# Optimization experiments

Hardware: AMD Instinct MI355X
Metric: run time of the kernel (lower is better)

Reference implementation:

```python
import jax, jax.numpy as jnp
import numpy as np

B, NP, NR = 4, 2048, 10
EDGE_F = 32
EMB = 64          # emb_features == out_features (required for layer stacking)
ESM_EMB = 64
HEADS = 16
NUM_LAYERS = 4
LN_EPS = 1e-5


def _ln(x, g, b):
    mu = jnp.mean(x, axis=-1, keepdims=True)
    var = jnp.var(x, axis=-1, keepdims=True)
    return (x - mu) / jnp.sqrt(var + LN_EPS) * g + b


def setup_inputs() -> dict:
    key = jax.random.key(0)
    ks = jax.random.split(key, 32)
    s = 0.05  # xavier-ish scale for weights
    inp = {
        "pep_feat": jax.random.normal(ks[0], (B, NP, 27 + 1280), jnp.float32),
        "rec_feat": jax.random.normal(ks[1], (B, NP, NR, 42 + 1280), jnp.float32),
        "edge_feat": jax.random.normal(ks[2], (B, NP, NR, EDGE_F), jnp.float32),
        # embedding weights (torch Linear convention: y = x @ W.T)
        "W_rec_esm": jax.random.normal(ks[3], (ESM_EMB, 1280), jnp.float32) * s,
        "W_pep_esm": jax.random.normal(ks[4], (ESM_EMB, 1280), jnp.float32) * s,
        "W_pep_emb": jax.random.normal(ks[5], (EMB, 27 + ESM_EMB), jnp.float32) * s,
        "W_rec_emb": jax.random.normal(ks[6], (EMB, 21 + ESM_EMB), jnp.float32) * s,
        "W_edge_emb": jax.random.normal(ks[7], (EMB, EDGE_F), jnp.float32) * s,
        "pep_ln_g": jnp.ones((EMB,), jnp.float32),
        "pep_ln_b": jnp.zeros((EMB,), jnp.float32),
        "rec_ln_g": jnp.ones((EMB,), jnp.float32),
        "rec_ln_b": jnp.zeros((EMB,), jnp.float32),
        # stacked GraphAttention layer params [L, ...]
        "ga_Wp": jax.random.normal(ks[8], (NUM_LAYERS, EMB, EMB), jnp.float32) * s,
        "ga_bp": jnp.zeros((NUM_LAYERS, EMB), jnp.float32),
        "ga_Wr": jax.random.normal(ks[9], (NUM_LAYERS, EMB, 2 * EMB), jnp.float32) * s,
        "ga_br": jnp.zeros((NUM_LAYERS, EMB), jnp.float32),
        "ga_Wv": jax.random.normal(ks[10], (NUM_LAYERS, EMB, 2 * EMB), jnp.float32) * s,
        "ga_bv": jnp.zeros((NUM_LAYERS, EMB), jnp.float32),
        # self-attention pooling: LN + MLP [64 -> 64 -> 32 -> 16 heads], no biases
        "pool_ln_g": jnp.ones((EMB,), jnp.float32),
        "pool_ln_b": jnp.zeros((EMB,), jnp.float32),
        "pool_W0": jax.random.normal(ks[11], (EMB, EMB), jnp.float32) * s,
        "pool_W1": jax.random.normal(ks[12], (EMB // 2, EMB), jnp.float32) * s,
        "pool_W2": jax.random.normal(ks[13], (HEADS, EMB // 2), jnp.float32) * s,
        # final projection
        "mlp_W": jax.random.normal(ks[14], (EMB // 2, EMB), jnp.float32) * s,
        "mlp_b": jnp.zeros((EMB // 2,), jnp.float32),
    }
    return inp


def _forward(pep_feat, rec_feat, edge_feat, W_rec_esm, W_pep_esm, W_pep_emb,
             W_rec_emb, W_edge_emb, pep_ln_g, pep_ln_b, rec_ln_g, rec_ln_b,
             ga_Wp, ga_bp, ga_Wr, ga_br, ga_Wv, ga_bv,
             pool_ln_g, pool_ln_b, pool_W0, pool_W1, pool_W2, mlp_W, mlp_b):
    # --- embeddings ---
    rec_esm = rec_feat[..., 42:] @ W_rec_esm.T                       # [B,NP,10,ESM]
    pep_esm = pep_feat[..., -1280:] @ W_pep_esm.T                    # [B,NP,ESM]
    rec = jnp.concatenate([rec_feat[..., :21], rec_esm], axis=-1) @ W_rec_emb.T
    pep = jnp.concatenate([pep_feat[..., :27], pep_esm], axis=-1) @ W_pep_emb.T
    edge = edge_feat @ W_edge_emb.T                                  # [B,NP,10,EMB]
    pep = _ln(pep, pep_ln_g, pep_ln_b)
    rec = _ln(rec, rec_ln_g, rec_ln_b)

    inv_sqrt_d = 1.0 / np.sqrt(EMB).astype(np.float32)
    rec_edge = jnp.concatenate([rec, edge], axis=-1)                 # [B,NP,10,2*EMB]
    # --- stacked GraphAttention layers (dropout = eval-mode identity) ---
    for l in range(NUM_LAYERS):
        q = pep @ ga_Wp[l].T + ga_bp[l]                              # [B,NP,EMB]
        key = rec_edge @ ga_Wr[l].T + ga_br[l]                       # [B,NP,10,EMB]
        val = rec_edge @ ga_Wv[l].T + ga_bv[l]                       # [B,NP,10,EMB]
        logit = jnp.einsum('bpd,bprd->bpr', q, key) * inv_sqrt_d     # [B,NP,10]
        attn = jax.nn.softmax(logit, axis=-1)
        pep = q + jnp.einsum('bpr,bprd->bpd', attn, val)             # [B,NP,EMB]

    # --- self-attention pooling (note: softmax applied twice, as in source) ---
    d = _ln(pep, pool_ln_g, pool_ln_b)                               # [B,NP,EMB]
    h = jnp.tanh(d @ pool_W0.T)
    h = jnp.tanh(h @ pool_W1.T)
    logits = h @ pool_W2.T                                           # [B,NP,HEADS]
    a = jax.nn.softmax(logits, axis=1)
    a = jax.nn.softmax(a, axis=1)
    attended = jnp.einsum('bsh,bsd->bhd', a, d)                      # [B,HEADS,EMB]
    pooled = attended.mean(axis=1)                                   # [B,EMB]
    return pooled @ mlp_W.T + mlp_b                                  # [B,EMB//2]


def reference(pep_feat, rec_feat, edge_feat, W_rec_esm, W_pep_esm, W_pep_emb,
              W_rec_emb, W_edge_emb, pep_ln_g, pep_ln_b, rec_ln_g, rec_ln_b,
              ga_Wp, ga_bp, ga_Wr, ga_br, ga_Wv, ga_bv,
              pool_ln_g, pool_ln_b, pool_W0, pool_W1, pool_W2, mlp_W, mlp_b):
    return _forward(pep_feat, rec_feat, edge_feat, W_rec_esm, W_pep_esm, W_pep_emb,
                    W_rec_emb, W_edge_emb, pep_ln_g, pep_ln_b, rec_ln_g, rec_ln_b,
                    ga_Wp, ga_bp, ga_Wr, ga_br, ga_Wv, ga_bv,
                    pool_ln_g, pool_ln_b, pool_W0, pool_W1, pool_W2, mlp_W, mlp_b)
```

## Files before the change

### kernel.cpp

```cpp
#include <hip/hip_runtime.h>
#include <hip/hip_bf16.h>


typedef __attribute__((ext_vector_type(8))) short bf16x8;
typedef __attribute__((ext_vector_type(4))) float f32x4;

#define MFMA(a, b, c) __builtin_amdgcn_mfma_f32_16x16x32_bf16((a), (b), (c), 0, 0, 0)

#define WB_REC_OFF   0
#define WB_PEP_OFF   83968
#define WB_EDGE_OFF  167936
#define WB_P_OFF     169984
#define WB_R_OFF     186368
#define WB_V_OFF     219136
#define WB_W0_OFF    251904
#define WB_W1_OFF    256000
#define WB_W2_OFF    258048
#define WB_TOTAL     258560

__device__ __forceinline__ unsigned short f2bf(float x) {
  __hip_bfloat16 h = __float2bfloat16(x);
  return __builtin_bit_cast(unsigned short, h);
}
__device__ __forceinline__ float bf2f(unsigned short u) {
  unsigned int t = ((unsigned int)u) << 16;
  return __builtin_bit_cast(float, t);
}
__device__ __forceinline__ bf16x8 loadBc(const unsigned short* base, int chunk, int lane) {
  return *(const bf16x8*)(base + ((size_t)chunk * 64 + lane) * 8);
}
__device__ __forceinline__ float tanhf_fast(float x) {
  float e = __expf(2.f * x);
  return 1.f - 2.f / (e + 1.f);
}

__global__ __launch_bounds__(256) void k_pack(
    const float* __restrict__ Wresm, const float* __restrict__ Wpesm,
    const float* __restrict__ Wre, const float* __restrict__ Wpe,
    const float* __restrict__ Wedge, const float* __restrict__ Wp,
    const float* __restrict__ Wr, const float* __restrict__ Wv,
    const float* __restrict__ W0, const float* __restrict__ W1,
    const float* __restrict__ W2, unsigned short* __restrict__ WB) {
  const int t = blockIdx.x * 256 + threadIdx.x;
  if (t >= WB_TOTAL) return;
  float v = 0.f;
  if (t < WB_EDGE_OFF) {
    bool isPep = (t >= WB_PEP_OFF);
    int u = isPep ? (t - WB_PEP_OFF) : t;
    int j = u & 7, lane = (u >> 3) & 63, n = (u >> 9) & 3, kc = u >> 11;
    int k = kc * 32 + ((lane >> 4) << 3) + j;
    int col = n * 16 + (lane & 15);
    if (kc < 40) {
      const float* wemb = isPep ? (Wpe + col * 91 + 27) : (Wre + col * 85 + 21);
      const float* wesm = isPep ? Wpesm : Wresm;
      float s = 0.f;
#pragma unroll 8
      for (int e = 0; e < 64; ++e) s += wemb[e] * wesm[e * 1280 + k];
      v = s;
    } else {
      int kl = k - 1280;
      if (isPep) v = (kl < 27) ? Wpe[col * 91 + kl] : 0.f;
      else       v = (kl < 21) ? Wre[col * 85 + kl] : 0.f;
    }
  } else if (t < WB_P_OFF) {
    int u = t - WB_EDGE_OFF;
    int j = u & 7, lane = (u >> 3) & 63, n = (u >> 9) & 3;
    v = Wedge[(n * 16 + (lane & 15)) * 32 + ((lane >> 4) << 3) + j];
  } else if (t < WB_R_OFF) {
    int u = t - WB_P_OFF;
    int l = u >> 12, w = u & 4095;
    int j = w & 7, lane = (w >> 3) & 63, n = (w >> 9) & 3, kc = w >> 11;
    int o = kc * 32 + ((lane >> 4) << 3) + j;
    int d = n * 16 + (lane & 15);
    v = Wp[l * 4096 + d * 64 + o];
  } else if (t < WB_V_OFF) {
    int u = t - WB_R_OFF;
    int l = u >> 13, w = u & 8191;
    int j = w & 7, lane = (w >> 3) & 63, c = (w >> 9) & 15;
    int kc = c >> 3, n = c & 7;
    int o = kc * 32 + ((lane >> 4) << 3) + j;
    int k = n * 16 + (lane & 15);
    v = Wr[l * 8192 + o * 128 + k];
  } else if (t < WB_W0_OFF) {
    int u = t - WB_V_OFF;
    int l = u >> 13, w = u & 8191;
    int j = w & 7, lane = (w >> 3) & 63, n = (w >> 9) & 3, kc = w >> 11;
    int k = kc * 32 + ((lane >> 4) << 3) + j;
    int d = n * 16 + (lane & 15);
    v = Wv[l * 8192 + d * 128 + k];
  } else if (t < WB_W1_OFF) {
    int u = t - WB_W0_OFF;
    int j = u & 7, lane = (u >> 3) & 63, c = u >> 9;
    int kc = c >> 2, n = c & 3;
    v = W0[(n * 16 + (lane & 15)) * 64 + kc * 32 + ((lane >> 4) << 3) + j];
  } else if (t < WB_W2_OFF) {
    int u = t - WB_W1_OFF;
    int j = u & 7, lane = (u >> 3) & 63, c = u >> 9;
    int kc = c >> 1, n = c & 1;
    v = W1[(n * 16 + (lane & 15)) * 64 + kc * 32 + ((lane >> 4) << 3) + j];
  } else {
    int u = t - WB_W2_OFF;
    int j = u & 7, lane = (u >> 3) & 63;
    v = W2[(lane & 15) * 32 + ((lane >> 4) << 3) + j];
  }
  WB[t] = f2bf(v);
}

__global__ __launch_bounds__(256) void k_emb(
    const float* __restrict__ rec_feat, const float* __restrict__ edge_feat,
    const float* __restrict__ pep_feat, const unsigned short* __restrict__ WB,
    const float* __restrict__ rec_g, const float* __restrict__ rec_b,
    const float* __restrict__ pep_g, const float* __restrict__ pep_b,
    unsigned short* __restrict__ rec_edge, unsigned short* __restrict__ pep_out) {
  __shared__ unsigned short stg4[4][2][16][128];
  const int tid = threadIdx.x;
  const int w = tid >> 6;
  const int lane = tid & 63;
  const int quad = lane >> 4, lr = lane & 15;
  const int tile = blockIdx.x * 4 + w;
  const bool isPep = (tile >= 5120);
  const int brow = (isPep ? tile - 5120 : tile) * 16;
  const float* __restrict__ src = isPep ? pep_feat : rec_feat;
  const int rowlen = isPep ? 1307 : 1322;
  const int head = isPep ? 27 : 42;
  const unsigned short* WBb = WB + (isPep ? WB_PEP_OFF : WB_REC_OFF);
  unsigned short (*stg)[16][128] = stg4[w];

  const f32x4 fz = {0.f, 0.f, 0.f, 0.f};
  f32x4 acc[4] = {fz, fz, fz, fz};

  float lx[16], ly[16];

  auto loadg = [&](int g) {
    if (!isPep) {
#pragma unroll
      for (int i = 0; i < 16; ++i) {
        const float2 v =
            *(const float2*)(src + (size_t)(brow + i) * 1322 + 42 + g * 128 + lane * 2);
        lx[i] = v.x; ly[i] = v.y;
      }
    } else {
#pragma unroll
      for (int i = 0; i < 16; ++i) {
        const float* p = src + (size_t)(brow + i) * 1307 + 27 + g * 128 + lane * 2;
        lx[i] = p[0]; ly[i] = p[1];
      }
    }
  };
  auto writeg = [&](int b) {
#pragma unroll
    for (int i = 0; i < 16; ++i) {
      const unsigned u = (unsigned)f2bf(lx[i]) | ((unsigned)f2bf(ly[i]) << 16);
      *(unsigned*)((char*)&stg[b][i][0] +
                   ((((lane >> 2) ^ i) << 4) | ((lane & 3) << 2))) = u;
    }
  };
  auto frag = [&](int b, int kc) -> bf16x8 {
    return *(const bf16x8*)((const char*)&stg[b][lr][0] +
                            ((((kc << 2) | quad) ^ lr) << 4));
  };

  loadg(0); writeg(0);
  int buf = 0;
  for (int g = 0; g < 10; ++g) {
    bf16x8 bb[16];
#pragma unroll
    for (int m = 0; m < 16; ++m) bb[m] = loadBc(WBb, g * 16 + m, lane);
    if (g < 9) loadg(g + 1);
#pragma unroll
    for (int c = 0; c < 4; ++c) {
      const bf16x8 a = frag(buf, c);
#pragma unroll
      for (int n = 0; n < 4; ++n) acc[n] = MFMA(a, bb[c * 4 + n], acc[n]);
    }
    if (g < 9) writeg(buf ^ 1);
    buf ^= 1;
  }
  {
    const float* p = src + (size_t)(brow + lr) * rowlen + quad * 8;
    bf16x8 a;
    if (!isPep) {
#pragma unroll
      for (int m = 0; m < 4; ++m) {
        const float2 v = *(const float2*)(p + 2 * m);
        a[2 * m] = (short)f2bf(v.x); a[2 * m + 1] = (short)f2bf(v.y);
      }
    } else {
#pragma unroll
      for (int j = 0; j < 8; ++j) a[j] = (short)f2bf(p[j]);
    }
#pragma unroll
    for (int n = 0; n < 4; ++n)
      acc[n] = MFMA(a, loadBc(WBb, 160 + n, lane), acc[n]);
  }

  float s[4], sq[4];
#pragma unroll
  for (int i = 0; i < 4; ++i) {
    s[i] = acc[0][i] + acc[1][i] + acc[2][i] + acc[3][i];
    sq[i] = acc[0][i] * acc[0][i] + acc[1][i] * acc[1][i] +
            acc[2][i] * acc[2][i] + acc[3][i] * acc[3][i];
  }
#pragma unroll
  for (int msk = 1; msk < 16; msk <<= 1) {
#pragma unroll
    for (int i = 0; i < 4; ++i) {
      s[i] += __shfl_xor(s[i], msk);
      sq[i] += __shfl_xor(sq[i], msk);
    }
  }
  const float* gp = isPep ? pep_g : rec_g;
  const float* bp = isPep ? pep_b : rec_b;
  float gv[4], bvl[4];
#pragma unroll
  for (int n = 0; n < 4; ++n) { gv[n] = gp[lr + 16 * n]; bvl[n] = bp[lr + 16 * n]; }

  if (!isPep) {
    f32x4 acce[4] = {fz, fz, fz, fz};
    {
      const float* p = edge_feat + (size_t)(brow + lr) * 32 + quad * 8;
      const float4 f0 = *(const float4*)(p);
      const float4 f1 = *(const float4*)(p + 4);
      bf16x8 a;
#pragma unroll
      for (int j = 0; j < 4; ++j) { a[j] = (short)f2bf(f0[j]); a[4 + j] = (short)f2bf(f1[j]); }
#pragma unroll
      for (int n = 0; n < 4; ++n) acce[n] = MFMA(a, loadBc(WB + WB_EDGE_OFF, n, lane), acce[n]);
    }
#pragma unroll
    for (int i = 0; i < 4; ++i) {
      const float mean = s[i] * (1.f / 64.f);
      const float var = sq[i] * (1.f / 64.f) - mean * mean;
      const float rstd = rsqrtf(var + 1e-5f);
      unsigned short* dst = rec_edge + (size_t)(brow + quad * 4 + i) * 128;
#pragma unroll
      for (int n = 0; n < 4; ++n) {
        dst[lr + 16 * n] = f2bf((acc[n][i] - mean) * rstd * gv[n] + bvl[n]);
        dst[64 + lr + 16 * n] = f2bf(acce[n][i]);
      }
    }
  } else {
#pragma unroll
    for (int i = 0; i < 4; ++i) {
      const float mean = s[i] * (1.f / 64.f);
      const float var = sq[i] * (1.f / 64.f) - mean * mean;
      const float rstd = rsqrtf(var + 1e-5f);
      unsigned short* dst = pep_out + (size_t)(brow + quad * 4 + i) * 64;
#pragma unroll
      for (int n = 0; n < 4; ++n)
        dst[lr + 16 * n] = f2bf((acc[n][i] - mean) * rstd * gv[n] + bvl[n]);
    }
  }
}

__global__ __launch_bounds__(256) void k_ga(
    const unsigned short* __restrict__ rec_edge, const unsigned short* __restrict__ pep_bf,
    const unsigned short* __restrict__ WB,
    const float* __restrict__ ga_bp, const float* __restrict__ ga_bv,
    const float* __restrict__ pool_g, const float* __restrict__ pool_b,
    float* __restrict__ dbuf, float* __restrict__ logitsT) {
  __shared__ unsigned short pep_s[1024];
  __shared__ unsigned short q_s[1024];
  __shared__ __align__(16) unsigned short zs[2048];
  __shared__ float bias_s[512];
  __shared__ float lgp[4][10][17];
  __shared__ float redp[4][2][16];
  __shared__ float oap[4][16][68];

  const int tid = threadIdx.x;
  const int w = tid >> 6;
  const int lane = tid & 63;
  const int quad = lane >> 4, lr = lane & 15;
  const int swz = lr & 7;
  const int pbase = blockIdx.x * 16;
  const int mycol = lr + 16 * w;
  const f32x4 fz = {0.f, 0.f, 0.f, 0.f};

  bias_s[tid] = ga_bp[tid & 255];
  bias_s[256 + tid] = ga_bv[tid & 255];
  if (tid < 128) {
    const int p = tid >> 3, gg = tid & 7;
    const bf16x8 v = *(const bf16x8*)(pep_bf + (size_t)(pbase + p) * 64 + gg * 8);
    *(bf16x8*)(pep_s + p * 64 + ((gg ^ (p & 7)) << 3)) = v;
  }
  const unsigned short* reb =
      rec_edge + (size_t)(pbase + lr) * 1280 + w * 32 + quad * 8;
  bf16x8 rfs[10];
#pragma unroll
  for (int r = 0; r < 10; ++r) rfs[r] = *(const bf16x8*)(reb + r * 128);
  __syncthreads();

  auto bwrite = [&](unsigned short* buf, int p, int col, unsigned short val) {
    buf[p * 64 + ((((col >> 3)) ^ (p & 7)) << 3) + (col & 7)] = val;
  };
  auto bfrag = [&](const unsigned short* buf, int kc) -> bf16x8 {
    return *(const bf16x8*)(buf + lr * 64 + ((((kc << 2) + quad) ^ swz) << 3));
  };

  f32x4 pcur;
  for (int l = 0; l < 4; ++l) {
    const unsigned short* WBp = WB + WB_P_OFF + l * 4096;
    const unsigned short* WBr = WB + WB_R_OFF + l * 8192;
    const unsigned short* WBv = WB + WB_V_OFF + l * 8192;

    f32x4 qa = fz;
    qa = MFMA(bfrag(pep_s, 0), loadBc(WBp, w, lane), qa);
    qa = MFMA(bfrag(pep_s, 1), loadBc(WBp, 4 + w, lane), qa);
    const float bpv = bias_s[l * 64 + mycol];
#pragma unroll
    for (int i = 0; i < 4; ++i) qa[i] += bpv;
#pragma unroll
    for (int i = 0; i < 4; ++i) bwrite(q_s, quad * 4 + i, mycol, f2bf(qa[i]));
    __syncthreads();

    const bf16x8 aq0 = bfrag(q_s, 0), aq1 = bfrag(q_s, 1);
    f32x4 za0 = fz, za1 = fz;
    za0 = MFMA(aq0, loadBc(WBr, 2 * w, lane), za0);
    za0 = MFMA(aq1, loadBc(WBr, 8 + 2 * w, lane), za0);
    za1 = MFMA(aq0, loadBc(WBr, 2 * w + 1, lane), za1);
    za1 = MFMA(aq1, loadBc(WBr, 9 + 2 * w, lane), za1);
#pragma unroll
    for (int i = 0; i < 4; ++i) {
      const int p = quad * 4 + i;
      const int k0 = 16 * (2 * w) + lr, k1 = 16 * (2 * w + 1) + lr;
      zs[p * 128 + ((((k0 >> 3) ^ (p & 7)) << 3) | (k0 & 7))] = f2bf(za0[i]);
      zs[p * 128 + ((((k1 >> 3) ^ (p & 7)) << 3) | (k1 & 7))] = f2bf(za1[i]);
    }
    float zfw[8];
    {
      const bf16x8 z8 = *(const bf16x8*)(zs + lr * 128 + (((quad + 4 * w) ^ swz) << 3));
#pragma unroll
      for (int j = 0; j < 8; ++j) zfw[j] = bf2f((unsigned short)z8[j]);
    }
#pragma unroll
    for (int r = 0; r < 10; ++r) {
      float part = 0.f;
#pragma unroll
      for (int j = 0; j < 8; ++j) part += bf2f((unsigned short)rfs[r][j]) * zfw[j];
      part += __shfl_xor(part, 16);
      part += __shfl_xor(part, 32);
      if (quad == 0) lgp[w][r][lr] = part;
    }
    __syncthreads();
    float lg[10];
#pragma unroll
    for (int r = 0; r < 10; ++r)
      lg[r] = (lgp[0][r][lr] + lgp[1][r][lr] + lgp[2][r][lr] + lgp[3][r][lr]) * 0.125f;
    float mx = lg[0];
#pragma unroll
    for (int r = 1; r < 10; ++r) mx = fmaxf(mx, lg[r]);
    float ssum = 0.f;
#pragma unroll
    for (int r = 0; r < 10; ++r) { lg[r] = __expf(lg[r] - mx); ssum += lg[r]; }
    const float inv = 1.f / ssum;
#pragma unroll
    for (int r = 0; r < 10; ++r) lg[r] *= inv;
    float wsacc[8] = {};
#pragma unroll
    for (int r = 0; r < 10; ++r)
#pragma unroll
      for (int j = 0; j < 8; ++j)
        wsacc[j] += lg[r] * bf2f((unsigned short)rfs[r][j]);
    bf16x8 wf;
#pragma unroll
    for (int j = 0; j < 8; ++j) wf[j] = (short)f2bf(wsacc[j]);
    f32x4 oa[4];
#pragma unroll
    for (int n = 0; n < 4; ++n) oa[n] = MFMA(wf, loadBc(WBv, w * 4 + n, lane), fz);
#pragma unroll
    for (int n = 0; n < 4; ++n)
#pragma unroll
      for (int i = 0; i < 4; ++i)
        oap[w][quad * 4 + i][n * 16 + lr] = oa[n][i];
    __syncthreads();
    const float bvv = bias_s[256 + l * 64 + mycol];
#pragma unroll
    for (int i = 0; i < 4; ++i) {
      const int p = quad * 4 + i;
      const float o = oap[0][p][mycol] + oap[1][p][mycol] +
                      oap[2][p][mycol] + oap[3][p][mycol];
      pcur[i] = qa[i] + o + bvv;
    }
#pragma unroll
    for (int i = 0; i < 4; ++i) bwrite(pep_s, quad * 4 + i, mycol, f2bf(pcur[i]));
    __syncthreads();
  }

  {
    float s[4], sq[4];
#pragma unroll
    for (int i = 0; i < 4; ++i) { s[i] = pcur[i]; sq[i] = pcur[i] * pcur[i]; }
#pragma unroll
    for (int msk = 1; msk < 16; msk <<= 1) {
#pragma unroll
      for (int i = 0; i < 4; ++i) {
        s[i] += __shfl_xor(s[i], msk);
        sq[i] += __shfl_xor(sq[i], msk);
      }
    }
    if (lr == 0) {
#pragma unroll
      for (int i = 0; i < 4; ++i) {
        redp[w][0][quad * 4 + i] = s[i];
        redp[w][1][quad * 4 + i] = sq[i];
      }
    }
    __syncthreads();
    const float gv = pool_g[mycol], bv2 = pool_b[mycol];
    float d[4];
    float* zf32 = (float*)zs;
#pragma unroll
    for (int i = 0; i < 4; ++i) {
      const int p = quad * 4 + i;
      const float sf = redp[0][0][p] + redp[1][0][p] + redp[2][0][p] + redp[3][0][p];
      const float sqf = redp[0][1][p] + redp[1][1][p] + redp[2][1][p] + redp[3][1][p];
      const float mean = sf * (1.f / 64.f);
      const float var = sqf * (1.f / 64.f) - mean * mean;
      const float rstd = rsqrtf(var + 1e-5f);
      d[i] = (pcur[i] - mean) * rstd * gv + bv2;
      zf32[p * 64 + mycol] = d[i];
      bwrite(q_s, p, mycol, f2bf(d[i]));
    }
    __syncthreads();
    {
      const float4 v = *(const float4*)(&zf32[tid * 4]);
      *(float4*)(dbuf + (size_t)pbase * 64 + tid * 4) = v;
    }
    if (w == 0) {
      const bf16x8 ad0 = bfrag(q_s, 0), ad1 = bfrag(q_s, 1);
      f32x4 h0[4] = {fz, fz, fz, fz};
#pragma unroll
      for (int n = 0; n < 4; ++n) {
        h0[n] = MFMA(ad0, loadBc(WB + WB_W0_OFF, n, lane), h0[n]);
        h0[n] = MFMA(ad1, loadBc(WB + WB_W0_OFF, 4 + n, lane), h0[n]);
      }
#pragma unroll
      for (int n = 0; n < 4; ++n)
#pragma unroll
        for (int i = 0; i < 4; ++i)
          bwrite(q_s, quad * 4 + i, lr + 16 * n, f2bf(tanhf_fast(h0[n][i])));
      const bf16x8 ah00 = bfrag(q_s, 0), ah01 = bfrag(q_s, 1);
      f32x4 h1[2] = {fz, fz};
#pragma unroll
      for (int n = 0; n < 2; ++n) {
        h1[n] = MFMA(ah00, loadBc(WB + WB_W1_OFF, n, lane), h1[n]);
        h1[n] = MFMA(ah01, loadBc(WB + WB_W1_OFF, 2 + n, lane), h1[n]);
      }
#pragma unroll
      for (int n = 0; n < 2; ++n)
#pragma unroll
        for (int i = 0; i < 4; ++i)
          bwrite(q_s, quad * 4 + i, lr + 16 * n, f2bf(tanhf_fast(h1[n][i])));
      const bf16x8 ah1 = bfrag(q_s, 0);
      f32x4 lac = MFMA(ah1, loadBc(WB + WB_W2_OFF, 0, lane), fz);
      const int b = pbase >> 11, sx0 = pbase & 2047;
#pragma unroll
      for (int i = 0; i < 4; ++i)
        logitsT[(size_t)(b * 16 + lr) * 2048 + sx0 + quad * 4 + i] = lac[i];
    }
  }
}

__global__ __launch_bounds__(256) void k_pool2(
    const float* __restrict__ logitsT, const float* __restrict__ dbuf,
    float* __restrict__ attp) {
  __shared__ float sh[2048];
  __shared__ float red[8];
  __shared__ float part[16][64];
  const int blk = blockIdx.x;
  const int bh = blk >> 2, q = blk & 3;
  const int b = bh >> 4;
  const int tid = threadIdx.x, lane = tid & 63, wid = tid >> 6;
  const float* lrow = logitsT + (size_t)bh * 2048;

  float m = -1e30f;
  for (int sx = tid; sx < 2048; sx += 256) {
    float v = lrow[sx];
    sh[sx] = v;
    m = fmaxf(m, v);
  }
#pragma unroll
  for (int msk = 1; msk < 64; msk <<= 1) m = fmaxf(m, __shfl_xor(m, msk));
  if (lane == 0) red[wid] = m;
  __syncthreads();
  m = fmaxf(fmaxf(red[0], red[1]), fmaxf(red[2], red[3]));

  float s1 = 0.f;
  for (int sx = tid; sx < 2048; sx += 256) {
    float e = __expf(sh[sx] - m);
    sh[sx] = e;
    s1 += e;
  }
#pragma unroll
  for (int msk = 1; msk < 64; msk <<= 1) s1 += __shfl_xor(s1, msk);
  __syncthreads();
  if (lane == 0) red[4 + wid] = s1;
  __syncthreads();
  s1 = red[4] + red[5] + red[6] + red[7];
  const float invS1 = 1.f / s1;

  float s2 = 0.f;
  for (int sx = tid; sx < 2048; sx += 256) {
    float e2 = __expf((sh[sx] - 1.f) * invS1);
    sh[sx] = e2;
    s2 += e2;
  }
#pragma unroll
  for (int msk = 1; msk < 64; msk <<= 1) s2 += __shfl_xor(s2, msk);
  __syncthreads();
  if (lane == 0) red[wid] = s2;
  __syncthreads();
  s2 = red[0] + red[1] + red[2] + red[3];
  const float invS2 = 1.f / s2;

  const int d16 = tid & 15, sxg = tid >> 4;
  float4 a4 = {0.f, 0.f, 0.f, 0.f};
  const float* db = dbuf + (size_t)b * 2048 * 64 + d16 * 4;
#pragma unroll 4
  for (int sx = q * 512 + sxg; sx < (q + 1) * 512; sx += 16) {
    const float w = sh[sx];
    const float4 v = *(const float4*)(db + (size_t)sx * 64);
    a4.x += w * v.x; a4.y += w * v.y; a4.z += w * v.z; a4.w += w * v.w;
  }
  *(float4*)(&part[sxg][d16 * 4]) = a4;
  __syncthreads();
  if (tid < 64) {
    float s = 0.f;
#pragma unroll
    for (int g2 = 0; g2 < 16; ++g2) s += part[g2][tid];
    attp[(size_t)(bh * 4 + q) * 64 + tid] = s * invS2;
  }
}

__global__ __launch_bounds__(256) void k_final(
    const float* __restrict__ attp, const float* __restrict__ W,
    const float* __restrict__ bias, float* __restrict__ out) {
  __shared__ float pooled[4][64];
  const int tid = threadIdx.x;
  {
    const int b = tid >> 6, d = tid & 63;
    float s = 0.f;
#pragma unroll
    for (int hq = 0; hq < 64; ++hq) s += attp[((size_t)b * 64 + hq) * 64 + d];
    pooled[b][d] = s * (1.f / 16.f);
  }
  __syncthreads();
  if (tid < 128) {
    const int b = tid >> 5, j = tid & 31;
    float s = bias[j];
#pragma unroll
    for (int d2 = 0; d2 < 64; ++d2) s += pooled[b][d2] * W[j * 64 + d2];
    out[b * 32 + j] = s;
  }
}

extern "C" void kernel_launch(void* const* d_in, const int* in_sizes, int n_in,
                              void* d_out, int out_size, void* d_ws, size_t ws_size,
                              hipStream_t stream) {
  const float* pep_feat = (const float*)d_in[0];
  const float* rec_feat = (const float*)d_in[1];
  const float* edge_feat = (const float*)d_in[2];
  const float* W_rec_esm = (const float*)d_in[3];
  const float* W_pep_esm = (const float*)d_in[4];
  const float* W_pep_emb = (const float*)d_in[5];
  const float* W_rec_emb = (const float*)d_in[6];
  const float* W_edge_emb = (const float*)d_in[7];
  const float* pep_ln_g = (const float*)d_in[8];
  const float* pep_ln_b = (const float*)d_in[9];
  const float* rec_ln_g = (const float*)d_in[10];
  const float* rec_ln_b = (const float*)d_in[11];
  const float* ga_Wp = (const float*)d_in[12];
  const float* ga_bp = (const float*)d_in[13];
  const float* ga_Wr = (const float*)d_in[14];
  const float* ga_br = (const float*)d_in[15];
  const float* ga_Wv = (const float*)d_in[16];
  const float* ga_bv = (const float*)d_in[17];
  const float* pool_ln_g = (const float*)d_in[18];
  const float* pool_ln_b = (const float*)d_in[19];
  const float* pool_W0 = (const float*)d_in[20];
  const float* pool_W1 = (const float*)d_in[21];
  const float* pool_W2 = (const float*)d_in[22];
  const float* mlp_W = (const float*)d_in[23];
  const float* mlp_b = (const float*)d_in[24];
  float* out = (float*)d_out;
  (void)ga_br;
  (void)ws_size; (void)in_sizes; (void)n_in; (void)out_size;

  char* ws = (char*)d_ws;
  unsigned short* WB = (unsigned short*)(ws);
  unsigned short* rec_edge = (unsigned short*)(ws + 524288);
  unsigned short* pep_bf = (unsigned short*)(ws + 21495808);
  float* dbuf = (float*)(ws + 22544384);
  float* logitsT = (float*)(ws + 24641536);
  float* attp = (float*)(ws + 25165824);

  k_pack<<<1010, 256, 0, stream>>>(W_rec_esm, W_pep_esm, W_rec_emb, W_pep_emb,
                                   W_edge_emb, ga_Wp, ga_Wr, ga_Wv,
                                   pool_W0, pool_W1, pool_W2, WB);
  k_emb<<<1408, 256, 0, stream>>>(rec_feat, edge_feat, pep_feat, WB,
                                  rec_ln_g, rec_ln_b, pep_ln_g, pep_ln_b,
                                  rec_edge, pep_bf);
  k_ga<<<512, 256, 0, stream>>>(rec_edge, pep_bf, WB, ga_bp, ga_bv,
                                pool_ln_g, pool_ln_b, dbuf, logitsT);
  k_pool2<<<256, 256, 0, stream>>>(logitsT, dbuf, attp);
  k_final<<<1, 256, 0, stream>>>(attp, mlp_W, mlp_b, out);
}
```

Baseline: 176.9 us.

## Restructure embedding GEMM to block-cooperative 64-row staging with coalesced loads

The embedding kernel now has each 256-thread block stage a 64-row by 320-column chunk of the ESM features into shared memory, using loads that are contiguous across threads and span rows, in four passes with block-wide barriers. Previously each wave staged its own 16-row tile in double-buffered 128-column slices. The aim is more coalesced global reads of the large fp32 feature tensor and fewer weight fragment reloads per pass. In exchange it adds __syncthreads barriers and drops the overlap between loading and MFMA work. The larger LDS footprint may also reduce occupancy.

```diff
diff --git a/kernel.cpp b/kernel.cpp
--- a/kernel.cpp
+++ b/kernel.cpp
@@ -112,72 +112,80 @@
     const float* __restrict__ rec_g, const float* __restrict__ rec_b,
     const float* __restrict__ pep_g, const float* __restrict__ pep_b,
     unsigned short* __restrict__ rec_edge, unsigned short* __restrict__ pep_out) {
-  __shared__ unsigned short stg4[4][2][16][128];
+  __shared__ unsigned short stg[64 * 320];
   const int tid = threadIdx.x;
   const int w = tid >> 6;
   const int lane = tid & 63;
   const int quad = lane >> 4, lr = lane & 15;
-  const int tile = blockIdx.x * 4 + w;
-  const bool isPep = (tile >= 5120);
-  const int brow = (isPep ? tile - 5120 : tile) * 16;
+  const bool isPep = (blockIdx.x >= 1280);
+  const int brow = (isPep ? (int)blockIdx.x - 1280 : (int)blockIdx.x) * 64;
+  const int myrow = 16 * w + lr;
   const float* __restrict__ src = isPep ? pep_feat : rec_feat;
   const int rowlen = isPep ? 1307 : 1322;
   const int head = isPep ? 27 : 42;
   const unsigned short* WBb = WB + (isPep ? WB_PEP_OFF : WB_REC_OFF);
-  unsigned short (*stg)[16][128] = stg4[w];
 
   const f32x4 fz = {0.f, 0.f, 0.f, 0.f};
   f32x4 acc[4] = {fz, fz, fz, fz};
 
-  float lx[16], ly[16];
-
-  auto loadg = [&](int g) {
-    if (!isPep) {
-#pragma unroll
-      for (int i = 0; i < 16; ++i) {
-        const float2 v =
-            *(const float2*)(src + (size_t)(brow + i) * 1322 + 42 + g * 128 + lane * 2);
-        lx[i] = v.x; ly[i] = v.y;
+  auto loadb = [&](float2 (&ld)[8], int q, int b) {
+#pragma unroll
+    for (int j = 0; j < 8; ++j) {
+      const int f = tid + 256 * (b * 8 + j);
+      const int row = f / 160, cp = f - row * 160;
+      const float* p = src + (size_t)(brow + row) * rowlen + head + q * 320 + cp * 2;
+      if (!isPep) {
+        ld[j] = *(const float2*)p;
+      } else {
+        ld[j].x = p[0]; ld[j].y = p[1];
       }
-    } else {
-#pragma unroll
-      for (int i = 0; i < 16; ++i) {
-        const float* p = src + (size_t)(brow + i) * 1307 + 27 + g * 128 + lane * 2;
-        lx[i] = p[0]; ly[i] = p[1];
-      }
     }
   };
-  auto writeg = [&](int b) {
-#pragma unroll
-    for (int i = 0; i < 16; ++i) {
-      const unsigned u = (unsigned)f2bf(lx[i]) | ((unsigned)f2bf(ly[i]) << 16);
-      *(unsigned*)((char*)&stg[b][i][0] +
-                   ((((lane >> 2) ^ i) << 4) | ((lane & 3) << 2))) = u;
+  auto writeb = [&](float2 (&ld)[8], int b) {
+#pragma unroll
+    for (int j = 0; j < 8; ++j) {
+      const int f = tid + 256 * (b * 8 + j);
+      const int row = f / 160, cp = f - row * 160;
+      const int u = cp >> 2;
+      const unsigned pk = (unsigned)f2bf(ld[j].x) | ((unsigned)f2bf(ld[j].y) << 16);
+      *(unsigned*)((char*)stg + row * 640 + ((u ^ (row & 7)) << 4) + ((cp & 3) << 2)) = pk;
     }
   };
-  auto frag = [&](int b, int kc) -> bf16x8 {
-    return *(const bf16x8*)((const char*)&stg[b][lr][0] +
-                            ((((kc << 2) | quad) ^ lr) << 4));
+  auto frag = [&](int g) -> bf16x8 {
+    return *(const bf16x8*)((const char*)stg + myrow * 640 +
+                            ((((g << 2) | quad) ^ (myrow & 7)) << 4));
   };
 
-  loadg(0); writeg(0);
-  int buf = 0;
-  for (int g = 0; g < 10; ++g) {
-    bf16x8 bb[16];
-#pragma unroll
-    for (int m = 0; m < 16; ++m) bb[m] = loadBc(WBb, g * 16 + m, lane);
-    if (g < 9) loadg(g + 1);
-#pragma unroll
-    for (int c = 0; c < 4; ++c) {
-      const bf16x8 a = frag(buf, c);
-#pragma unroll
-      for (int n = 0; n < 4; ++n) acc[n] = MFMA(a, bb[c * 4 + n], acc[n]);
-    }
-    if (g < 9) writeg(buf ^ 1);
-    buf ^= 1;
-  }
+  for (int q = 0; q < 4; ++q) {
+    {
+      float2 lda[8], ldb[8];
+      loadb(lda, q, 0);
+      loadb(ldb, q, 1);
+      writeb(lda, 0);
+      loadb(lda, q, 2);
+      writeb(ldb, 1);
+      loadb(ldb, q, 3);
+      writeb(lda, 2);
+      loadb(lda, q, 4);
+      writeb(ldb, 3);
+      writeb(lda, 4);
+    }
+    __syncthreads();
+#pragma unroll
+    for (int g = 0; g < 10; ++g) {
+      bf16x8 bb[4];
+#pragma unroll
+      for (int n = 0; n < 4; ++n)
+        bb[n] = loadBc(WBb, (q * 10 + g) * 4 + n, lane);
+      const bf16x8 a = frag(g);
+#pragma unroll
+      for (int n = 0; n < 4; ++n) acc[n] = MFMA(a, bb[n], acc[n]);
+    }
+    __syncthreads();
+  }
+
   {
-    const float* p = src + (size_t)(brow + lr) * rowlen + quad * 8;
+    const float* p = src + (size_t)(brow + myrow) * rowlen + quad * 8;
     bf16x8 a;
     if (!isPep) {
 #pragma unroll
@@ -218,7 +226,7 @@
   if (!isPep) {
     f32x4 acce[4] = {fz, fz, fz, fz};
     {
-      const float* p = edge_feat + (size_t)(brow + lr) * 32 + quad * 8;
+      const float* p = edge_feat + (size_t)(brow + myrow) * 32 + quad * 8;
       const float4 f0 = *(const float4*)(p);
       const float4 f1 = *(const float4*)(p + 4);
       bf16x8 a;
@@ -232,7 +240,7 @@
       const float mean = s[i] * (1.f / 64.f);
       const float var = sq[i] * (1.f / 64.f) - mean * mean;
       const float rstd = rsqrtf(var + 1e-5f);
-      unsigned short* dst = rec_edge + (size_t)(brow + quad * 4 + i) * 128;
+      unsigned short* dst = rec_edge + (size_t)(brow + 16 * w + quad * 4 + i) * 128;
 #pragma unroll
       for (int n = 0; n < 4; ++n) {
         dst[lr + 16 * n] = f2bf((acc[n][i] - mean) * rstd * gv[n] + bvl[n]);
@@ -245,7 +253,7 @@
       const float mean = s[i] * (1.f / 64.f);
       const float var = sq[i] * (1.f / 64.f) - mean * mean;
       const float rstd = rsqrtf(var + 1e-5f);
-      unsigned short* dst = pep_out + (size_t)(brow + quad * 4 + i) * 64;
+      unsigned short* dst = pep_out + (size_t)(brow + 16 * w + quad * 4 + i) * 64;
 #pragma unroll
       for (int n = 0; n < 4; ++n)
         dst[lr + 16 * n] = f2bf((acc[n][i] - mean) * rstd * gv[n] + bvl[n]);
```

Result: faster. 170.4 us (-3.7%).
